# Kernel optimization log

Hardware: AMD Instinct MI355X
Metric: run time of the kernel (lower is better)

Reference implementation:

```python
import jax, jax.numpy as jnp
import numpy as np

N = 50000
E = 800000
FEAT = 128
COND = 64
HID = 128
LAT = 64


def setup_inputs() -> dict:
    key = jax.random.key(0)
    ks = jax.random.split(key, 16)
    inp = {
        "feature": jax.random.normal(ks[0], (N, FEAT), jnp.float32),
        "condition": jax.random.normal(ks[1], (N, COND), jnp.float32),
        "edge_index": jax.random.randint(ks[2], (2, E), 0, N, jnp.int64 if jax.config.jax_enable_x64 else jnp.int32),
        "noise": jax.random.normal(ks[3], (N, LAT), jnp.float32),
        # GCNConv params (glorot-style scale)
        "W_f2h": jax.random.normal(ks[4], (FEAT, HID), jnp.float32) * (1.0 / np.sqrt(FEAT)),
        "b_f2h": jnp.zeros((HID,), jnp.float32),
        "W_c2h": jax.random.normal(ks[5], (COND, HID), jnp.float32) * (1.0 / np.sqrt(COND)),
        "b_c2h": jnp.zeros((HID,), jnp.float32),
        "W_h2h": jax.random.normal(ks[6], (2 * HID, HID), jnp.float32) * (1.0 / np.sqrt(2 * HID)),
        "b_h2h": jnp.zeros((HID,), jnp.float32),
        "W_mean": jax.random.normal(ks[7], (HID, LAT), jnp.float32) * (1.0 / np.sqrt(HID)),
        "b_mean": jnp.zeros((LAT,), jnp.float32),
        "W_logvar": jax.random.normal(ks[8], (HID, LAT), jnp.float32) * (1.0 / np.sqrt(HID)),
        "b_logvar": jnp.zeros((LAT,), jnp.float32),
    }
    return inp


def _gcn_norm(edge_index, n):
    # add self-loops, compute symmetric normalization deg^-1/2 * deg^-1/2
    loop = jnp.arange(n, dtype=edge_index.dtype)
    src = jnp.concatenate([edge_index[0], loop])
    dst = jnp.concatenate([edge_index[1], loop])
    deg = jax.ops.segment_sum(jnp.ones_like(src, jnp.float32), dst, num_segments=n)
    dinv = jnp.where(deg > 0, jax.lax.rsqrt(deg), 0.0)
    norm = dinv[src] * dinv[dst]  # [E+N]
    return src, dst, norm


def _gcn_conv(x, W, b, src, dst, norm, n):
    h = x @ W                                  # [N, out]
    msg = h[src] * norm[:, None]               # gather + scale, [E+N, out]
    out = jax.ops.segment_sum(msg, dst, num_segments=n)
    return out + b


def reference(feature, condition, edge_index, noise,
              W_f2h, b_f2h, W_c2h, b_c2h, W_h2h, b_h2h,
              W_mean, b_mean, W_logvar, b_logvar):
    n = feature.shape[0]
    src, dst, norm = _gcn_norm(edge_index, n)
    f2h = jnp.tanh(_gcn_conv(feature, W_f2h, b_f2h, src, dst, norm, n))
    c2h = jnp.tanh(_gcn_conv(condition, W_c2h, b_c2h, src, dst, norm, n))
    h = jnp.concatenate([f2h, c2h], axis=1)
    h = jnp.tanh(_gcn_conv(h, W_h2h, b_h2h, src, dst, norm, n))
    mean = _gcn_conv(h, W_mean, b_mean, src, dst, norm, n)
    logvar = _gcn_conv(h, W_logvar, b_logvar, src, dst, norm, n)
    z = noise * jnp.exp(0.5 * logvar) + mean
    return (z, mean, logvar)
```

## Files before the change

### kernel.cpp

```cpp
#include <hip/hip_runtime.h>
#include <math.h>

namespace {

constexpr int N = 50000;
constexpr int E = 800000;

typedef __attribute__((ext_vector_type(8))) short short8;
typedef __attribute__((ext_vector_type(4))) float f32x4;
typedef __attribute__((ext_vector_type(2))) float f32x2;


__device__ inline unsigned short f2bf(float f) {
  unsigned int b = __float_as_uint(f);
  unsigned int r = (b + 0x7fffu + ((b >> 16) & 1u)) >> 16;
  return (unsigned short)r;
}
__device__ inline float bf_lo(unsigned int u) { return __uint_as_float(u << 16); }
__device__ inline float bf_hi(unsigned int u) { return __uint_as_float(u & 0xffff0000u); }
__device__ inline unsigned int pack2(float a, float b) {
  return (unsigned int)f2bf(a) | ((unsigned int)f2bf(b) << 16);
}


__device__ inline unsigned int pack4_fp8(float a, float b, float c, float d) {
  int w = 0;
  w = __builtin_amdgcn_cvt_pk_fp8_f32(a, b, w, false);
  w = __builtin_amdgcn_cvt_pk_fp8_f32(c, d, w, true);
  return (unsigned int)w;
}
__device__ inline unsigned char f2fp8(float v) {
  return (unsigned char)(__builtin_amdgcn_cvt_pk_fp8_f32(v, v, 0, false) & 0xff);
}


__global__ void zero_int(int* p, int n) {
  int i = blockIdx.x * blockDim.x + threadIdx.x;
  if (i < n) p[i] = 0;
}

__global__ void count_deg_rank(const int* __restrict__ dst, int* __restrict__ cnt,
                               int* __restrict__ rank, int e) {
  int i = blockIdx.x * blockDim.x + threadIdx.x;
  if (i < e) rank[i] = atomicAdd(&cnt[dst[i]], 1);
}

__global__ void block_sums(const int* __restrict__ cnt, int* __restrict__ bsum, int n) {
  int tid = threadIdx.x;
  int i = blockIdx.x * 256 + tid;
  int v = (i < n) ? cnt[i] : 0;
  for (int off = 32; off > 0; off >>= 1) v += __shfl_down(v, off, 64);
  __shared__ int sred[4];
  if ((tid & 63) == 0) sred[tid >> 6] = v;
  __syncthreads();
  if (tid == 0) bsum[blockIdx.x] = sred[0] + sred[1] + sred[2] + sred[3];
}

__global__ void scan_bsums(int* bsum, int nb) {
  if (threadIdx.x == 0 && blockIdx.x == 0) {
    int run = 0;
    for (int b = 0; b < nb; ++b) { int t = bsum[b]; bsum[b] = run; run += t; }
  }
}

__global__ void scan_chunks(const int* __restrict__ cnt, const int* __restrict__ bsum,
                            int* __restrict__ row_ptr, int n) {
  __shared__ int s[256];
  int tid = threadIdx.x;
  int i = blockIdx.x * 256 + tid;
  int v = (i < n) ? cnt[i] : 0;
  s[tid] = v;
  __syncthreads();
  for (int d = 1; d < 256; d <<= 1) {
    int t = (tid >= d) ? s[tid - d] : 0;
    __syncthreads();
    s[tid] += t;
    __syncthreads();
  }
  if (i < n) {
    int excl = bsum[blockIdx.x] + s[tid] - v;
    row_ptr[i] = excl;
    if (i == n - 1) row_ptr[n] = excl + v;
  }
}

__global__ void compute_dinv(const int* __restrict__ cnt, float* __restrict__ dinv, int n) {
  int i = blockIdx.x * blockDim.x + threadIdx.x;
  if (i < n) dinv[i] = rsqrtf((float)(cnt[i] + 1));
}

__global__ __launch_bounds__(256) void scatter_xcd(const int* __restrict__ src,
                                                   const int* __restrict__ dst,
                                                   const int* __restrict__ rank,
                                                   const int* __restrict__ row_ptr,
                                                   int* __restrict__ csr_src) {
  constexpr int RANGE = (N + 7) / 8;
  int r = blockIdx.x & 7;
  int lo = r * RANGE;
  int hi = lo + RANGE;
  int nb = gridDim.x >> 3;
  int bi = blockIdx.x >> 3;
  for (int e = bi * 256 + threadIdx.x; e < E; e += nb * 256) {
    int d = dst[e];
    if (d >= lo && d < hi) {
      csr_src[row_ptr[d] + rank[e]] = src[e];
    }
  }
}


__global__ void cvt_cond(const float* __restrict__ in, const float* __restrict__ dinv,
                         unsigned char* __restrict__ out, int n) {
  int t = blockIdx.x * blockDim.x + threadIdx.x;
  if (t >= n * 8) return;
  int i = t >> 3, j = t & 7;
  float di = dinv[i];
  const float* s = in + (size_t)i * 64 + j * 8;
  float4 a = *(const float4*)s;
  float4 b = *(const float4*)(s + 4);
  uint2 o;
  o.x = pack4_fp8(di * a.x, di * a.y, di * a.z, di * a.w);
  o.y = pack4_fp8(di * b.x, di * b.y, di * b.z, di * b.w);
  *(uint2*)(out + (size_t)i * 192 + 128 + j * 8) = o;
}

__global__ void pack_w(const float* __restrict__ W1, int s1,
                       const float* __restrict__ W2, int s2, int split,
                       int ksteps, unsigned short* __restrict__ out) {
  int t = blockIdx.x * blockDim.x + threadIdx.x;
  int total = ksteps * 8 * 64;
  if (t >= total) return;
  int ks = t >> 9;
  int ct = (t >> 6) & 7;
  int l = t & 63;
  int k0 = ks * 32 + ((l >> 4) << 3);
  int col = ct * 16 + (l & 15);
  const float* src;
  int c;
  if (col < split) { src = W1 + col; c = s1; }
  else { src = W2 + (col - split); c = s2; }
  unsigned short* o = out + (size_t)t * 8;
#pragma unroll
  for (int i = 0; i < 8; ++i) o[i] = f2bf(src[(size_t)(k0 + i) * c]);
}

__global__ void make_bcat(const float* __restrict__ bm, const float* __restrict__ bl,
                          float* __restrict__ bcat) {
  int j = threadIdx.x;
  if (j < 64) bcat[j] = bm[j];
  else if (j < 128) bcat[j] = bl[j - 64];
}


template <int K, int EPI, bool F32A, int OUT>
__global__ __launch_bounds__(256) void gemm_mfma(const void* __restrict__ Av, int lda,
                                                 const unsigned short* __restrict__ Wp,
                                                 const float* __restrict__ bias_or_scale,
                                                 void* __restrict__ Cv, int ldc, int n) {
  constexpr int KSTEPS = K / 32;
  int tid = threadIdx.x;
  int w = tid >> 6;
  int l = tid & 63;
  int r0 = blockIdx.x * 128 + w * 32;
  int arow = l & 15;
  int kgrp = l >> 4;

  f32x4 acc[2][8];
#pragma unroll
  for (int m = 0; m < 2; ++m)
#pragma unroll
    for (int ct = 0; ct < 8; ++ct) acc[m][ct] = (f32x4)(0.f);

  int ra0 = min(r0 + arow, n - 1);
  int ra1 = min(r0 + 16 + arow, n - 1);

#pragma unroll 1
  for (int ks = 0; ks < KSTEPS; ++ks) {
    short8 a0, a1;
    if (F32A) {
      const float* p0 = (const float*)Av + (size_t)ra0 * lda + kgrp * 8 + ks * 32;
      const float* p1 = (const float*)Av + (size_t)ra1 * lda + kgrp * 8 + ks * 32;
      float4 x0 = *(const float4*)p0, y0 = *(const float4*)(p0 + 4);
      float4 x1 = *(const float4*)p1, y1 = *(const float4*)(p1 + 4);
      unsigned int u[4];
      u[0] = pack2(x0.x, x0.y); u[1] = pack2(x0.z, x0.w);
      u[2] = pack2(y0.x, y0.y); u[3] = pack2(y0.z, y0.w);
      a0 = *(const short8*)u;
      u[0] = pack2(x1.x, x1.y); u[1] = pack2(x1.z, x1.w);
      u[2] = pack2(y1.x, y1.y); u[3] = pack2(y1.z, y1.w);
      a1 = *(const short8*)u;
    } else {
      a0 = *(const short8*)((const unsigned short*)Av + (size_t)ra0 * lda + kgrp * 8 + ks * 32);
      a1 = *(const short8*)((const unsigned short*)Av + (size_t)ra1 * lda + kgrp * 8 + ks * 32);
    }
    const short8* pb = (const short8*)Wp + (size_t)(ks * 8) * 64 + l;
#pragma unroll
    for (int ct = 0; ct < 8; ++ct) {
      short8 b = pb[ct * 64];
      acc[0][ct] = __builtin_amdgcn_mfma_f32_16x16x32_bf16(a0, b, acc[0][ct], 0, 0, 0);
      acc[1][ct] = __builtin_amdgcn_mfma_f32_16x16x32_bf16(a1, b, acc[1][ct], 0, 0, 0);
    }
  }

  int ccol = l & 15;
  int crow = (l >> 4) * 4;
#pragma unroll
  for (int ct = 0; ct < 8; ++ct) {
    int col = ct * 16 + ccol;
    float bv = (EPI == 1) ? bias_or_scale[col] : 0.f;
#pragma unroll
    for (int m = 0; m < 2; ++m) {
#pragma unroll
      for (int r = 0; r < 4; ++r) {
        int row = r0 + m * 16 + crow + r;
        if (row < n) {
          float v = acc[m][ct][r];
          if (EPI == 1) v = tanhf(v + bv);
          if (EPI == 2) v = v * bias_or_scale[row];
          if (OUT == 0)
            ((unsigned short*)Cv)[(size_t)row * ldc + col] = f2bf(v);
          else
            ((unsigned char*)Cv)[(size_t)row * ldc + col] = f2fp8(v);
        }
      }
    }
  }
}


#define ACC16_ADD_FP8(ACC, U)                                           \
  {                                                                     \
    f32x2 t0 = __builtin_amdgcn_cvt_pk_f32_fp8((int)U.x, false);        \
    f32x2 t1 = __builtin_amdgcn_cvt_pk_f32_fp8((int)U.x, true);         \
    f32x2 t2 = __builtin_amdgcn_cvt_pk_f32_fp8((int)U.y, false);        \
    f32x2 t3 = __builtin_amdgcn_cvt_pk_f32_fp8((int)U.y, true);         \
    f32x2 t4 = __builtin_amdgcn_cvt_pk_f32_fp8((int)U.z, false);        \
    f32x2 t5 = __builtin_amdgcn_cvt_pk_f32_fp8((int)U.z, true);         \
    f32x2 t6 = __builtin_amdgcn_cvt_pk_f32_fp8((int)U.w, false);        \
    f32x2 t7 = __builtin_amdgcn_cvt_pk_f32_fp8((int)U.w, true);         \
    ACC[0] += t0[0]; ACC[1] += t0[1]; ACC[2] += t1[0]; ACC[3] += t1[1]; \
    ACC[4] += t2[0]; ACC[5] += t2[1]; ACC[6] += t3[0]; ACC[7] += t3[1]; \
    ACC[8] += t4[0]; ACC[9] += t4[1]; ACC[10] += t5[0]; ACC[11] += t5[1]; \
    ACC[12] += t6[0]; ACC[13] += t6[1]; ACC[14] += t7[0]; ACC[15] += t7[1]; \
  }


__global__ __launch_bounds__(256) void prop192(const unsigned char* __restrict__ X,
                                               unsigned short* __restrict__ f2h_out,
                                               unsigned short* __restrict__ pc_out,
                                               const int* __restrict__ row_ptr,
                                               const int* __restrict__ csr_src,
                                               const float* __restrict__ dinv,
                                               const float* __restrict__ b_f2h, int n) {
  int wave = threadIdx.x >> 6;
  int wlane = threadIdx.x & 63;
  int rrow = wlane / 12;
  int wl = wlane - rrow * 12;
  if (rrow >= 5) return;
  int i = blockIdx.x * 20 + wave * 5 + rrow;
  if (i >= n) return;
  const uint4* X16 = (const uint4*)X;
  float di = dinv[i];
  float acc[16], accB[16];
#pragma unroll
  for (int j = 0; j < 16; ++j) { acc[j] = 0.f; accB[j] = 0.f; }
  {
    uint4 u = X16[(size_t)i * 12 + wl];
    ACC16_ADD_FP8(acc, u)
  }
  int e0 = row_ptr[i], e1 = row_ptr[i + 1];
  int e = e0;
  for (; e + 2 <= e1; e += 2) {
    int s0 = csr_src[e], s1 = csr_src[e + 1];
    uint4 u0 = X16[(size_t)s0 * 12 + wl];
    uint4 u1 = X16[(size_t)s1 * 12 + wl];
    ACC16_ADD_FP8(acc, u0)
    ACC16_ADD_FP8(accB, u1)
  }
  if (e < e1) {
    int s0 = csr_src[e];
    uint4 u0 = X16[(size_t)s0 * 12 + wl];
    ACC16_ADD_FP8(acc, u0)
  }
#pragma unroll
  for (int j = 0; j < 16; ++j) acc[j] += accB[j];

  if (wl < 8) {
    float out[16];
#pragma unroll
    for (int j = 0; j < 16; ++j) out[j] = tanhf(fmaf(di, acc[j], b_f2h[wl * 16 + j]));
    unsigned short* yp = f2h_out + (size_t)i * 256 + wl * 16;
    uint4 o0, o1;
    o0.x = pack2(out[0], out[1]); o0.y = pack2(out[2], out[3]);
    o0.z = pack2(out[4], out[5]); o0.w = pack2(out[6], out[7]);
    o1.x = pack2(out[8], out[9]); o1.y = pack2(out[10], out[11]);
    o1.z = pack2(out[12], out[13]); o1.w = pack2(out[14], out[15]);
    *(uint4*)yp = o0;
    *(uint4*)(yp + 8) = o1;
  } else {
    unsigned short* yp = pc_out + (size_t)i * 64 + (wl - 8) * 16;
    uint4 o0, o1;
    o0.x = pack2(di * acc[0], di * acc[1]); o0.y = pack2(di * acc[2], di * acc[3]);
    o0.z = pack2(di * acc[4], di * acc[5]); o0.w = pack2(di * acc[6], di * acc[7]);
    o1.x = pack2(di * acc[8], di * acc[9]); o1.y = pack2(di * acc[10], di * acc[11]);
    o1.z = pack2(di * acc[12], di * acc[13]); o1.w = pack2(di * acc[14], di * acc[15]);
    *(uint4*)yp = o0;
    *(uint4*)(yp + 8) = o1;
  }
}


__global__ __launch_bounds__(256) void prop128(const unsigned char* __restrict__ X,
                                               unsigned short* __restrict__ Y,
                                               const int* __restrict__ row_ptr,
                                               const int* __restrict__ csr_src,
                                               const float* __restrict__ dinv,
                                               const float* __restrict__ bias, int n) {
  int wl = threadIdx.x & 7;
  int rloc = threadIdx.x >> 3;
  int i = blockIdx.x * 32 + rloc;
  if (i >= n) return;
  const uint4* X16 = (const uint4*)X;
  float di = dinv[i];
  float acc[16], accB[16];
#pragma unroll
  for (int j = 0; j < 16; ++j) { acc[j] = 0.f; accB[j] = 0.f; }
  {
    uint4 u = X16[(size_t)i * 8 + wl];
    ACC16_ADD_FP8(acc, u)
  }
  int e0 = row_ptr[i], e1 = row_ptr[i + 1];
  int e = e0;
  for (; e + 2 <= e1; e += 2) {
    int s0 = csr_src[e], s1 = csr_src[e + 1];
    uint4 u0 = X16[(size_t)s0 * 8 + wl];
    uint4 u1 = X16[(size_t)s1 * 8 + wl];
    ACC16_ADD_FP8(acc, u0)
    ACC16_ADD_FP8(accB, u1)
  }
  if (e < e1) {
    int s0 = csr_src[e];
    uint4 u0 = X16[(size_t)s0 * 8 + wl];
    ACC16_ADD_FP8(acc, u0)
  }
#pragma unroll
  for (int j = 0; j < 16; ++j) acc[j] += accB[j];

  float out[16];
#pragma unroll
  for (int j = 0; j < 16; ++j) out[j] = tanhf(fmaf(di, acc[j], bias[wl * 16 + j]));
  unsigned short* yp = Y + (size_t)i * 128 + wl * 16;
  uint4 o0, o1;
  o0.x = pack2(out[0], out[1]); o0.y = pack2(out[2], out[3]);
  o0.z = pack2(out[4], out[5]); o0.w = pack2(out[6], out[7]);
  o1.x = pack2(out[8], out[9]); o1.y = pack2(out[10], out[11]);
  o1.z = pack2(out[12], out[13]); o1.w = pack2(out[14], out[15]);
  *(uint4*)yp = o0;
  *(uint4*)(yp + 8) = o1;
}


__global__ __launch_bounds__(256) void prop_fin(const unsigned char* __restrict__ X,
                                                const int* __restrict__ row_ptr,
                                                const int* __restrict__ csr_src,
                                                const float* __restrict__ dinv,
                                                const float* __restrict__ bcat,
                                                const float* __restrict__ noise,
                                                float* __restrict__ out, int n) {
  int wl = threadIdx.x & 7;
  int rloc = threadIdx.x >> 3;
  int i = blockIdx.x * 32 + rloc;
  if (i >= n) return;
  const uint4* X16 = (const uint4*)X;
  float di = dinv[i];
  float acc[16], accB[16];
#pragma unroll
  for (int j = 0; j < 16; ++j) { acc[j] = 0.f; accB[j] = 0.f; }
  {
    uint4 u = X16[(size_t)i * 8 + wl];
    ACC16_ADD_FP8(acc, u)
  }
  int e0 = row_ptr[i], e1 = row_ptr[i + 1];
  int e = e0;
  for (; e + 2 <= e1; e += 2) {
    int s0 = csr_src[e], s1 = csr_src[e + 1];
    uint4 u0 = X16[(size_t)s0 * 8 + wl];
    uint4 u1 = X16[(size_t)s1 * 8 + wl];
    ACC16_ADD_FP8(acc, u0)
    ACC16_ADD_FP8(accB, u1)
  }
  if (e < e1) {
    int s0 = csr_src[e];
    uint4 u0 = X16[(size_t)s0 * 8 + wl];
    ACC16_ADD_FP8(acc, u0)
  }
#pragma unroll
  for (int j = 0; j < 16; ++j) acc[j] += accB[j];

  float v[16];
#pragma unroll
  for (int j = 0; j < 16; ++j) v[j] = fmaf(di, acc[j], bcat[wl * 16 + j]);
  const float* nz = noise + (size_t)i * 64 + (wl & 3) * 16;
  float tt[16];
#pragma unroll
  for (int j = 0; j < 16; ++j) tt[j] = nz[j] * expf(0.5f * v[j]);
  int srcl = ((int)(threadIdx.x & 63) & ~7) + 4 + (wl & 3);
  float z[16];
#pragma unroll
  for (int j = 0; j < 16; ++j) z[j] = v[j] + __shfl(tt[j], srcl);

  size_t n64 = (size_t)n * 64;
  if (wl < 4) {
    float* zp = out + (size_t)i * 64 + wl * 16;
    *(float4*)zp = make_float4(z[0], z[1], z[2], z[3]);
    *(float4*)(zp + 4) = make_float4(z[4], z[5], z[6], z[7]);
    *(float4*)(zp + 8) = make_float4(z[8], z[9], z[10], z[11]);
    *(float4*)(zp + 12) = make_float4(z[12], z[13], z[14], z[15]);
    float* mp = out + n64 + (size_t)i * 64 + wl * 16;
    *(float4*)mp = make_float4(v[0], v[1], v[2], v[3]);
    *(float4*)(mp + 4) = make_float4(v[4], v[5], v[6], v[7]);
    *(float4*)(mp + 8) = make_float4(v[8], v[9], v[10], v[11]);
    *(float4*)(mp + 12) = make_float4(v[12], v[13], v[14], v[15]);
  } else {
    float* lp = out + 2 * n64 + (size_t)i * 64 + (wl - 4) * 16;
    *(float4*)lp = make_float4(v[0], v[1], v[2], v[3]);
    *(float4*)(lp + 4) = make_float4(v[4], v[5], v[6], v[7]);
    *(float4*)(lp + 8) = make_float4(v[8], v[9], v[10], v[11]);
    *(float4*)(lp + 12) = make_float4(v[12], v[13], v[14], v[15]);
  }
}

}

extern "C" void kernel_launch(void* const* d_in, const int* in_sizes, int n_in,
                              void* d_out, int out_size, void* d_ws, size_t ws_size,
                              hipStream_t stream) {
  const float* feature   = (const float*)d_in[0];
  const float* condition = (const float*)d_in[1];
  const int*   ei        = (const int*)d_in[2];
  const float* noise     = (const float*)d_in[3];
  const float* W_f2h     = (const float*)d_in[4];
  const float* b_f2h     = (const float*)d_in[5];
  const float* W_c2h     = (const float*)d_in[6];
  const float* b_c2h     = (const float*)d_in[7];
  const float* W_h2h     = (const float*)d_in[8];
  const float* b_h2h     = (const float*)d_in[9];
  const float* W_mean    = (const float*)d_in[10];
  const float* b_mean    = (const float*)d_in[11];
  const float* W_logvar  = (const float*)d_in[12];
  const float* b_logvar  = (const float*)d_in[13];

  const int* src = ei;
  const int* dst = ei + E;

  char* p = (char*)d_ws;
  auto alloc = [&](size_t bytes) {
    char* q = p;
    p += (bytes + 255) & ~(size_t)255;
    return q;
  };
  unsigned char*  buf192 = (unsigned char*)alloc((size_t)N * 192);
  unsigned char*  u2buf  = (unsigned char*)alloc((size_t)N * 128);
  unsigned char*  vbuf   = (unsigned char*)alloc((size_t)N * 128);
  unsigned short* catbuf = (unsigned short*)alloc((size_t)N * 256 * 2);
  unsigned short* Pcbf   = (unsigned short*)alloc((size_t)N * 64 * 2);
  unsigned short* hbuf   = (unsigned short*)alloc((size_t)N * 128 * 2);
  int*   cnt     = (int*)alloc((size_t)N * 4);
  int*   rank    = (int*)alloc((size_t)E * 4);
  int*   row_ptr = (int*)alloc((size_t)(N + 1) * 4);
  int*   csr_src = (int*)alloc((size_t)E * 4);
  int*   bsum    = (int*)alloc(256 * 4);
  float* dinv    = (float*)alloc((size_t)N * 4);
  unsigned short* Wf2h_p = (unsigned short*)alloc(4 * 512 * 8 * 2);
  unsigned short* Wc2h_p = (unsigned short*)alloc(2 * 512 * 8 * 2);
  unsigned short* Wh2h_p = (unsigned short*)alloc(8 * 512 * 8 * 2);
  unsigned short* Wcat_p = (unsigned short*)alloc(4 * 512 * 8 * 2);
  float* bcat    = (float*)alloc(128 * 4);
  (void)ws_size; (void)in_sizes; (void)n_in; (void)out_size;

  int nb = (N + 255) / 256;

  zero_int<<<nb, 256, 0, stream>>>(cnt, N);
  count_deg_rank<<<(E + 255) / 256, 256, 0, stream>>>(dst, cnt, rank, E);
  block_sums<<<nb, 256, 0, stream>>>(cnt, bsum, N);
  scan_bsums<<<1, 64, 0, stream>>>(bsum, nb);
  scan_chunks<<<nb, 256, 0, stream>>>(cnt, bsum, row_ptr, N);
  compute_dinv<<<(N + 255) / 256, 256, 0, stream>>>(cnt, dinv, N);
  scatter_xcd<<<1024, 256, 0, stream>>>(src, dst, rank, row_ptr, csr_src);

  cvt_cond<<<(N * 8 + 255) / 256, 256, 0, stream>>>(condition, dinv, buf192, N);
  pack_w<<<(4 * 512 + 255) / 256, 256, 0, stream>>>(W_f2h, 128, nullptr, 0, 128, 4, Wf2h_p);
  pack_w<<<(2 * 512 + 255) / 256, 256, 0, stream>>>(W_c2h, 128, nullptr, 0, 128, 2, Wc2h_p);
  pack_w<<<(8 * 512 + 255) / 256, 256, 0, stream>>>(W_h2h, 128, nullptr, 0, 128, 8, Wh2h_p);
  pack_w<<<(4 * 512 + 255) / 256, 256, 0, stream>>>(W_mean, 64, W_logvar, 64, 64, 4, Wcat_p);
  make_bcat<<<1, 128, 0, stream>>>(b_mean, b_logvar, bcat);

  int ggrid = (N + 127) / 128;

  gemm_mfma<128, 2, true, 1><<<ggrid, 256, 0, stream>>>(feature, 128, Wf2h_p, dinv, buf192, 192, N);
  prop192<<<(N + 19) / 20, 256, 0, stream>>>(buf192, catbuf, Pcbf, row_ptr, csr_src, dinv, b_f2h, N);
  gemm_mfma<64, 1, false, 0><<<ggrid, 256, 0, stream>>>(Pcbf, 64, Wc2h_p, b_c2h, catbuf + 128, 256, N);
  gemm_mfma<256, 2, false, 1><<<ggrid, 256, 0, stream>>>(catbuf, 256, Wh2h_p, dinv, u2buf, 128, N);
  prop128<<<(N + 31) / 32, 256, 0, stream>>>(u2buf, hbuf, row_ptr, csr_src, dinv, b_h2h, N);
  gemm_mfma<128, 2, false, 1><<<ggrid, 256, 0, stream>>>(hbuf, 128, Wcat_p, dinv, vbuf, 128, N);
  prop_fin<<<(N + 31) / 32, 256, 0, stream>>>(vbuf, row_ptr, csr_src, dinv, bcat, noise,
                                              (float*)d_out, N);
}
```

Before: 283.5 us.

## Assign one wavefront per node and split neighbor edges across lane groups

Each graph propagation kernel now maps one 64-lane wave to one destination node. Lane groups stride over the node's self-loop plus incoming edges in parallel, and partial sums are combined with cross-lane shuffles. Previously one node was handled by a small group of lanes that walked all edges serially. The first-layer buffer is padded from 192 to 256 bytes per row so 16 lanes cover a full row, at the cost of extra zeroed padding and a wider gather. The goal is more memory-level parallelism per node; the cost is shuffle reductions, fewer nodes per block, and idle lanes when nodes have low degree.

```diff
diff --git a/kernel.cpp b/kernel.cpp
--- a/kernel.cpp
+++ b/kernel.cpp
@@ -16,8 +16,6 @@
   unsigned int r = (b + 0x7fffu + ((b >> 16) & 1u)) >> 16;
   return (unsigned short)r;
 }
-__device__ inline float bf_lo(unsigned int u) { return __uint_as_float(u << 16); }
-__device__ inline float bf_hi(unsigned int u) { return __uint_as_float(u & 0xffff0000u); }
 __device__ inline unsigned int pack2(float a, float b) {
   return (unsigned int)f2bf(a) | ((unsigned int)f2bf(b) << 16);
 }
@@ -121,7 +119,8 @@
   uint2 o;
   o.x = pack4_fp8(di * a.x, di * a.y, di * a.z, di * a.w);
   o.y = pack4_fp8(di * b.x, di * b.y, di * b.z, di * b.w);
-  *(uint2*)(out + (size_t)i * 192 + 128 + j * 8) = o;
+  *(uint2*)(out + (size_t)i * 256 + 128 + j * 8) = o;
+  *(uint2*)(out + (size_t)i * 256 + 192 + j * 8) = make_uint2(0u, 0u);
 }
 
 __global__ void pack_w(const float* __restrict__ W1, int s1,
@@ -245,46 +244,53 @@
   }
 
 
-__global__ __launch_bounds__(256) void prop192(const unsigned char* __restrict__ X,
+__global__ __launch_bounds__(256) void prop256(const unsigned char* __restrict__ X,
                                                unsigned short* __restrict__ f2h_out,
                                                unsigned short* __restrict__ pc_out,
                                                const int* __restrict__ row_ptr,
                                                const int* __restrict__ csr_src,
                                                const float* __restrict__ dinv,
                                                const float* __restrict__ b_f2h, int n) {
-  int wave = threadIdx.x >> 6;
-  int wlane = threadIdx.x & 63;
-  int rrow = wlane / 12;
-  int wl = wlane - rrow * 12;
-  if (rrow >= 5) return;
-  int i = blockIdx.x * 20 + wave * 5 + rrow;
+  int lane = threadIdx.x & 63;
+  int wl = lane & 15;
+  int g = lane >> 4;
+  int i = blockIdx.x * 4 + (threadIdx.x >> 6);
   if (i >= n) return;
   const uint4* X16 = (const uint4*)X;
   float di = dinv[i];
+  int e0 = row_ptr[i];
+  int total = row_ptr[i + 1] - e0 + 1;
+  int itc = (total + 3) >> 2;
   float acc[16], accB[16];
 #pragma unroll
   for (int j = 0; j < 16; ++j) { acc[j] = 0.f; accB[j] = 0.f; }
-  {
-    uint4 u = X16[(size_t)i * 12 + wl];
-    ACC16_ADD_FP8(acc, u)
-  }
-  int e0 = row_ptr[i], e1 = row_ptr[i + 1];
-  int e = e0;
-  for (; e + 2 <= e1; e += 2) {
-    int s0 = csr_src[e], s1 = csr_src[e + 1];
-    uint4 u0 = X16[(size_t)s0 * 12 + wl];
-    uint4 u1 = X16[(size_t)s1 * 12 + wl];
-    ACC16_ADD_FP8(acc, u0)
-    ACC16_ADD_FP8(accB, u1)
-  }
-  if (e < e1) {
-    int s0 = csr_src[e];
-    uint4 u0 = X16[(size_t)s0 * 12 + wl];
-    ACC16_ADD_FP8(acc, u0)
-  }
-#pragma unroll
-  for (int j = 0; j < 16; ++j) acc[j] += accB[j];
-
+  int it = 0;
+  for (; it + 2 <= itc; it += 2) {
+    int itemA = it * 4 + g;
+    int itemB = itemA + 4;
+    bool aA = itemA < total;
+    bool aB = itemB < total;
+    int sA = i, sB = i;
+    if (aA && itemA > 0) sA = csr_src[e0 + itemA - 1];
+    if (aB) sB = csr_src[e0 + itemB - 1];
+    if (aA) { uint4 u = X16[(size_t)sA * 16 + wl]; ACC16_ADD_FP8(acc, u) }
+    if (aB) { uint4 u = X16[(size_t)sB * 16 + wl]; ACC16_ADD_FP8(accB, u) }
+  }
+  if (it < itc) {
+    int item = it * 4 + g;
+    bool a = item < total;
+    int s = i;
+    if (a && item > 0) s = csr_src[e0 + item - 1];
+    if (a) { uint4 u = X16[(size_t)s * 16 + wl]; ACC16_ADD_FP8(acc, u) }
+  }
+#pragma unroll
+  for (int j = 0; j < 16; ++j) {
+    float v = acc[j] + accB[j];
+    v += __shfl_xor(v, 16);
+    v += __shfl_xor(v, 32);
+    acc[j] = v;
+  }
+  if (g != 0) return;
   if (wl < 8) {
     float out[16];
 #pragma unroll
@@ -297,7 +303,7 @@
     o1.z = pack2(out[12], out[13]); o1.w = pack2(out[14], out[15]);
     *(uint4*)yp = o0;
     *(uint4*)(yp + 8) = o1;
-  } else {
+  } else if (wl < 12) {
     unsigned short* yp = pc_out + (size_t)i * 64 + (wl - 8) * 16;
     uint4 o0, o1;
     o0.x = pack2(di * acc[0], di * acc[1]); o0.y = pack2(di * acc[2], di * acc[3]);
@@ -316,36 +322,47 @@
                                                const int* __restrict__ csr_src,
                                                const float* __restrict__ dinv,
                                                const float* __restrict__ bias, int n) {
-  int wl = threadIdx.x & 7;
-  int rloc = threadIdx.x >> 3;
-  int i = blockIdx.x * 32 + rloc;
+  int lane = threadIdx.x & 63;
+  int wl = lane & 7;
+  int g = lane >> 3;
+  int i = blockIdx.x * 4 + (threadIdx.x >> 6);
   if (i >= n) return;
   const uint4* X16 = (const uint4*)X;
   float di = dinv[i];
+  int e0 = row_ptr[i];
+  int total = row_ptr[i + 1] - e0 + 1;
+  int itc = (total + 7) >> 3;
   float acc[16], accB[16];
 #pragma unroll
   for (int j = 0; j < 16; ++j) { acc[j] = 0.f; accB[j] = 0.f; }
-  {
-    uint4 u = X16[(size_t)i * 8 + wl];
-    ACC16_ADD_FP8(acc, u)
-  }
-  int e0 = row_ptr[i], e1 = row_ptr[i + 1];
-  int e = e0;
-  for (; e + 2 <= e1; e += 2) {
-    int s0 = csr_src[e], s1 = csr_src[e + 1];
-    uint4 u0 = X16[(size_t)s0 * 8 + wl];
-    uint4 u1 = X16[(size_t)s1 * 8 + wl];
-    ACC16_ADD_FP8(acc, u0)
-    ACC16_ADD_FP8(accB, u1)
-  }
-  if (e < e1) {
-    int s0 = csr_src[e];
-    uint4 u0 = X16[(size_t)s0 * 8 + wl];
-    ACC16_ADD_FP8(acc, u0)
-  }
-#pragma unroll
-  for (int j = 0; j < 16; ++j) acc[j] += accB[j];
-
+  int it = 0;
+  for (; it + 2 <= itc; it += 2) {
+    int itemA = it * 8 + g;
+    int itemB = itemA + 8;
+    bool aA = itemA < total;
+    bool aB = itemB < total;
+    int sA = i, sB = i;
+    if (aA && itemA > 0) sA = csr_src[e0 + itemA - 1];
+    if (aB) sB = csr_src[e0 + itemB - 1];
+    if (aA) { uint4 u = X16[(size_t)sA * 8 + wl]; ACC16_ADD_FP8(acc, u) }
+    if (aB) { uint4 u = X16[(size_t)sB * 8 + wl]; ACC16_ADD_FP8(accB, u) }
+  }
+  if (it < itc) {
+    int item = it * 8 + g;
+    bool a = item < total;
+    int s = i;
+    if (a && item > 0) s = csr_src[e0 + item - 1];
+    if (a) { uint4 u = X16[(size_t)s * 8 + wl]; ACC16_ADD_FP8(acc, u) }
+  }
+#pragma unroll
+  for (int j = 0; j < 16; ++j) {
+    float v = acc[j] + accB[j];
+    v += __shfl_xor(v, 8);
+    v += __shfl_xor(v, 16);
+    v += __shfl_xor(v, 32);
+    acc[j] = v;
+  }
+  if (g != 0) return;
   float out[16];
 #pragma unroll
   for (int j = 0; j < 16; ++j) out[j] = tanhf(fmaf(di, acc[j], bias[wl * 16 + j]));
@@ -367,36 +384,47 @@
                                                 const float* __restrict__ bcat,
                                                 const float* __restrict__ noise,
                                                 float* __restrict__ out, int n) {
-  int wl = threadIdx.x & 7;
-  int rloc = threadIdx.x >> 3;
-  int i = blockIdx.x * 32 + rloc;
+  int lane = threadIdx.x & 63;
+  int wl = lane & 7;
+  int g = lane >> 3;
+  int i = blockIdx.x * 4 + (threadIdx.x >> 6);
   if (i >= n) return;
   const uint4* X16 = (const uint4*)X;
   float di = dinv[i];
+  int e0 = row_ptr[i];
+  int total = row_ptr[i + 1] - e0 + 1;
+  int itc = (total + 7) >> 3;
   float acc[16], accB[16];
 #pragma unroll
   for (int j = 0; j < 16; ++j) { acc[j] = 0.f; accB[j] = 0.f; }
-  {
-    uint4 u = X16[(size_t)i * 8 + wl];
-    ACC16_ADD_FP8(acc, u)
-  }
-  int e0 = row_ptr[i], e1 = row_ptr[i + 1];
-  int e = e0;
-  for (; e + 2 <= e1; e += 2) {
-    int s0 = csr_src[e], s1 = csr_src[e + 1];
-    uint4 u0 = X16[(size_t)s0 * 8 + wl];
-    uint4 u1 = X16[(size_t)s1 * 8 + wl];
-    ACC16_ADD_FP8(acc, u0)
-    ACC16_ADD_FP8(accB, u1)
-  }
-  if (e < e1) {
-    int s0 = csr_src[e];
-    uint4 u0 = X16[(size_t)s0 * 8 + wl];
-    ACC16_ADD_FP8(acc, u0)
-  }
-#pragma unroll
-  for (int j = 0; j < 16; ++j) acc[j] += accB[j];
-
+  int it = 0;
+  for (; it + 2 <= itc; it += 2) {
+    int itemA = it * 8 + g;
+    int itemB = itemA + 8;
+    bool aA = itemA < total;
+    bool aB = itemB < total;
+    int sA = i, sB = i;
+    if (aA && itemA > 0) sA = csr_src[e0 + itemA - 1];
+    if (aB) sB = csr_src[e0 + itemB - 1];
+    if (aA) { uint4 u = X16[(size_t)sA * 8 + wl]; ACC16_ADD_FP8(acc, u) }
+    if (aB) { uint4 u = X16[(size_t)sB * 8 + wl]; ACC16_ADD_FP8(accB, u) }
+  }
+  if (it < itc) {
+    int item = it * 8 + g;
+    bool a = item < total;
+    int s = i;
+    if (a && item > 0) s = csr_src[e0 + item - 1];
+    if (a) { uint4 u = X16[(size_t)s * 8 + wl]; ACC16_ADD_FP8(acc, u) }
+  }
+#pragma unroll
+  for (int j = 0; j < 16; ++j) {
+    float v = acc[j] + accB[j];
+    v += __shfl_xor(v, 8);
+    v += __shfl_xor(v, 16);
+    v += __shfl_xor(v, 32);
+    acc[j] = v;
+  }
+  if (g != 0) return;
   float v[16];
 #pragma unroll
   for (int j = 0; j < 16; ++j) v[j] = fmaf(di, acc[j], bcat[wl * 16 + j]);
@@ -404,7 +432,7 @@
   float tt[16];
 #pragma unroll
   for (int j = 0; j < 16; ++j) tt[j] = nz[j] * expf(0.5f * v[j]);
-  int srcl = ((int)(threadIdx.x & 63) & ~7) + 4 + (wl & 3);
+  int srcl = 4 + (wl & 3);
   float z[16];
 #pragma unroll
   for (int j = 0; j < 16; ++j) z[j] = v[j] + __shfl(tt[j], srcl);
@@ -459,7 +487,7 @@
     p += (bytes + 255) & ~(size_t)255;
     return q;
   };
-  unsigned char*  buf192 = (unsigned char*)alloc((size_t)N * 192);
+  unsigned char*  buf256 = (unsigned char*)alloc((size_t)N * 256);
   unsigned char*  u2buf  = (unsigned char*)alloc((size_t)N * 128);
   unsigned char*  vbuf   = (unsigned char*)alloc((size_t)N * 128);
   unsigned short* catbuf = (unsigned short*)alloc((size_t)N * 256 * 2);
@@ -488,7 +516,7 @@
   compute_dinv<<<(N + 255) / 256, 256, 0, stream>>>(cnt, dinv, N);
   scatter_xcd<<<1024, 256, 0, stream>>>(src, dst, rank, row_ptr, csr_src);
 
-  cvt_cond<<<(N * 8 + 255) / 256, 256, 0, stream>>>(condition, dinv, buf192, N);
+  cvt_cond<<<(N * 8 + 255) / 256, 256, 0, stream>>>(condition, dinv, buf256, N);
   pack_w<<<(4 * 512 + 255) / 256, 256, 0, stream>>>(W_f2h, 128, nullptr, 0, 128, 4, Wf2h_p);
   pack_w<<<(2 * 512 + 255) / 256, 256, 0, stream>>>(W_c2h, 128, nullptr, 0, 128, 2, Wc2h_p);
   pack_w<<<(8 * 512 + 255) / 256, 256, 0, stream>>>(W_h2h, 128, nullptr, 0, 128, 8, Wh2h_p);
@@ -496,13 +524,14 @@
   make_bcat<<<1, 128, 0, stream>>>(b_mean, b_logvar, bcat);
 
   int ggrid = (N + 127) / 128;
-
-  gemm_mfma<128, 2, true, 1><<<ggrid, 256, 0, stream>>>(feature, 128, Wf2h_p, dinv, buf192, 192, N);
-  prop192<<<(N + 19) / 20, 256, 0, stream>>>(buf192, catbuf, Pcbf, row_ptr, csr_src, dinv, b_f2h, N);
+  int pgrid = (N + 3) / 4;
+
+  gemm_mfma<128, 2, true, 1><<<ggrid, 256, 0, stream>>>(feature, 128, Wf2h_p, dinv, buf256, 256, N);
+  prop256<<<pgrid, 256, 0, stream>>>(buf256, catbuf, Pcbf, row_ptr, csr_src, dinv, b_f2h, N);
   gemm_mfma<64, 1, false, 0><<<ggrid, 256, 0, stream>>>(Pcbf, 64, Wc2h_p, b_c2h, catbuf + 128, 256, N);
   gemm_mfma<256, 2, false, 1><<<ggrid, 256, 0, stream>>>(catbuf, 256, Wh2h_p, dinv, u2buf, 128, N);
-  prop128<<<(N + 31) / 32, 256, 0, stream>>>(u2buf, hbuf, row_ptr, csr_src, dinv, b_h2h, N);
+  prop128<<<pgrid, 256, 0, stream>>>(u2buf, hbuf, row_ptr, csr_src, dinv, b_h2h, N);
   gemm_mfma<128, 2, false, 1><<<ggrid, 256, 0, stream>>>(hbuf, 128, Wcat_p, dinv, vbuf, 128, N);
-  prop_fin<<<(N + 31) / 32, 256, 0, stream>>>(vbuf, row_ptr, csr_src, dinv, bcat, noise,
-                                              (float*)d_out, N);
-}
+  prop_fin<<<pgrid, 256, 0, stream>>>(vbuf, row_ptr, csr_src, dinv, bcat, noise,
+                                      (float*)d_out, N);
+}
```

New measurement: 356.4 us. 1.26x slower.

## Rework CSR build: XCD-partitioned counting, fused scan+dinv, cursor-based scatter

Applied to the files above, without the earlier changes.

The degree-count kernel now uses XCD-partitioned atomics, so each destination range is handled by blocks on one XCD, and it no longer stores a per-edge rank array. The block-sum scan, chunk scan and dinv computation are merged into one kernel that computes each block's prefix in parallel and also sets a cursor array. The scatter step takes slots with atomics on that cursor instead of reading rank and row_ptr. This removes several launches and the E-sized rank traffic. In exchange, neighbor order within each CSR row becomes nondeterministic, which can change floating-point summation order.

```diff
diff --git a/kernel.cpp b/kernel.cpp
--- a/kernel.cpp
+++ b/kernel.cpp
@@ -16,8 +16,6 @@
   unsigned int r = (b + 0x7fffu + ((b >> 16) & 1u)) >> 16;
   return (unsigned short)r;
 }
-__device__ inline float bf_lo(unsigned int u) { return __uint_as_float(u << 16); }
-__device__ inline float bf_hi(unsigned int u) { return __uint_as_float(u & 0xffff0000u); }
 __device__ inline unsigned int pack2(float a, float b) {
   return (unsigned int)f2bf(a) | ((unsigned int)f2bf(b) << 16);
 }
@@ -39,10 +37,18 @@
   if (i < n) p[i] = 0;
 }
 
-__global__ void count_deg_rank(const int* __restrict__ dst, int* __restrict__ cnt,
-                               int* __restrict__ rank, int e) {
-  int i = blockIdx.x * blockDim.x + threadIdx.x;
-  if (i < e) rank[i] = atomicAdd(&cnt[dst[i]], 1);
+__global__ __launch_bounds__(256) void count_xcd(const int* __restrict__ dst,
+                                                 int* __restrict__ cnt) {
+  constexpr int RANGE = (N + 7) / 8;
+  int r = blockIdx.x & 7;
+  int lo = r * RANGE;
+  int hi = lo + RANGE;
+  int nb = gridDim.x >> 3;
+  int bi = blockIdx.x >> 3;
+  for (int e = bi * 256 + threadIdx.x; e < E; e += nb * 256) {
+    int d = dst[e];
+    if (d >= lo && d < hi) atomicAdd(&cnt[d], 1);
+  }
 }
 
 __global__ void block_sums(const int* __restrict__ cnt, int* __restrict__ bsum, int n) {
@@ -56,17 +62,18 @@
   if (tid == 0) bsum[blockIdx.x] = sred[0] + sred[1] + sred[2] + sred[3];
 }
 
-__global__ void scan_bsums(int* bsum, int nb) {
-  if (threadIdx.x == 0 && blockIdx.x == 0) {
-    int run = 0;
-    for (int b = 0; b < nb; ++b) { int t = bsum[b]; bsum[b] = run; run += t; }
-  }
-}
-
-__global__ void scan_chunks(const int* __restrict__ cnt, const int* __restrict__ bsum,
-                            int* __restrict__ row_ptr, int n) {
+__global__ void scan_chunks2(const int* __restrict__ cnt, const int* __restrict__ bsum,
+                             int nbk, int* __restrict__ row_ptr, int* __restrict__ cursor,
+                             float* __restrict__ dinv, int n) {
   __shared__ int s[256];
+  __shared__ int sred[4];
+  __shared__ int sprefix;
   int tid = threadIdx.x;
+  int pv = (tid < nbk && tid < (int)blockIdx.x) ? bsum[tid] : 0;
+  for (int off = 32; off > 0; off >>= 1) pv += __shfl_down(pv, off, 64);
+  if ((tid & 63) == 0) sred[tid >> 6] = pv;
+  __syncthreads();
+  if (tid == 0) sprefix = sred[0] + sred[1] + sred[2] + sred[3];
   int i = blockIdx.x * 256 + tid;
   int v = (i < n) ? cnt[i] : 0;
   s[tid] = v;
@@ -78,21 +85,17 @@
     __syncthreads();
   }
   if (i < n) {
-    int excl = bsum[blockIdx.x] + s[tid] - v;
+    int excl = sprefix + s[tid] - v;
     row_ptr[i] = excl;
+    cursor[i] = excl;
+    dinv[i] = rsqrtf((float)(v + 1));
     if (i == n - 1) row_ptr[n] = excl + v;
   }
-}
-
-__global__ void compute_dinv(const int* __restrict__ cnt, float* __restrict__ dinv, int n) {
-  int i = blockIdx.x * blockDim.x + threadIdx.x;
-  if (i < n) dinv[i] = rsqrtf((float)(cnt[i] + 1));
 }
 
 __global__ __launch_bounds__(256) void scatter_xcd(const int* __restrict__ src,
                                                    const int* __restrict__ dst,
-                                                   const int* __restrict__ rank,
-                                                   const int* __restrict__ row_ptr,
+                                                   int* __restrict__ cursor,
                                                    int* __restrict__ csr_src) {
   constexpr int RANGE = (N + 7) / 8;
   int r = blockIdx.x & 7;
@@ -103,7 +106,8 @@
   for (int e = bi * 256 + threadIdx.x; e < E; e += nb * 256) {
     int d = dst[e];
     if (d >= lo && d < hi) {
-      csr_src[row_ptr[d] + rank[e]] = src[e];
+      int pos = atomicAdd(&cursor[d], 1);
+      csr_src[pos] = src[e];
     }
   }
 }
@@ -466,7 +470,7 @@
   unsigned short* Pcbf   = (unsigned short*)alloc((size_t)N * 64 * 2);
   unsigned short* hbuf   = (unsigned short*)alloc((size_t)N * 128 * 2);
   int*   cnt     = (int*)alloc((size_t)N * 4);
-  int*   rank    = (int*)alloc((size_t)E * 4);
+  int*   cursor  = (int*)alloc((size_t)N * 4);
   int*   row_ptr = (int*)alloc((size_t)(N + 1) * 4);
   int*   csr_src = (int*)alloc((size_t)E * 4);
   int*   bsum    = (int*)alloc(256 * 4);
@@ -481,12 +485,10 @@
   int nb = (N + 255) / 256;
 
   zero_int<<<nb, 256, 0, stream>>>(cnt, N);
-  count_deg_rank<<<(E + 255) / 256, 256, 0, stream>>>(dst, cnt, rank, E);
+  count_xcd<<<1024, 256, 0, stream>>>(dst, cnt);
   block_sums<<<nb, 256, 0, stream>>>(cnt, bsum, N);
-  scan_bsums<<<1, 64, 0, stream>>>(bsum, nb);
-  scan_chunks<<<nb, 256, 0, stream>>>(cnt, bsum, row_ptr, N);
-  compute_dinv<<<(N + 255) / 256, 256, 0, stream>>>(cnt, dinv, N);
-  scatter_xcd<<<1024, 256, 0, stream>>>(src, dst, rank, row_ptr, csr_src);
+  scan_chunks2<<<nb, 256, 0, stream>>>(cnt, bsum, nb, row_ptr, cursor, dinv, N);
+  scatter_xcd<<<1024, 256, 0, stream>>>(src, dst, cursor, csr_src);
 
   cvt_cond<<<(N * 8 + 255) / 256, 256, 0, stream>>>(condition, dinv, buf192, N);
   pack_w<<<(4 * 512 + 255) / 256, 256, 0, stream>>>(W_f2h, 128, nullptr, 0, 128, 4, Wf2h_p);
```

Measured after the change: 283.7 us. No clear change (+0.1%).
